# Kernel tuning notes

Measured on AMD Instinct MI355X. Metric: run time of the kernel, lower is better.

## Reference

```python
import jax, jax.numpy as jnp
import numpy as np

OBS, ACT, EMB, HID, NQ = 512, 32, 512, 512, 32
B = 32768


def setup_inputs() -> dict:
    key = jax.random.key(0)
    ks = jax.random.split(key, 12)
    s_in = 1.0 / np.sqrt(OBS + ACT)
    s_emb = 1.0 / np.sqrt(EMB)
    s_hid = 1.0 / np.sqrt(HID)
    return {
        "observation": jax.random.normal(ks[0], (B, OBS), jnp.float32),
        "prev_action": jax.random.normal(ks[1], (B, ACT), jnp.float32),
        "hidden_state": jax.random.normal(ks[2], (HID,), jnp.float32),
        "cell_state": jax.random.normal(ks[3], (HID,), jnp.float32),
        "W1": jax.random.uniform(ks[4], (EMB, OBS + ACT), jnp.float32, -s_in, s_in),
        "b1": jax.random.uniform(ks[5], (EMB,), jnp.float32, -s_in, s_in),
        "W_ih": jax.random.uniform(ks[6], (4 * HID, EMB), jnp.float32, -s_hid, s_hid),
        "b_ih": jax.random.uniform(ks[7], (4 * HID,), jnp.float32, -s_hid, s_hid),
        "W_hh": jax.random.uniform(ks[8], (4 * HID, HID), jnp.float32, -s_hid, s_hid),
        "b_hh": jax.random.uniform(ks[9], (4 * HID,), jnp.float32, -s_hid, s_hid),
        "W2": jax.random.uniform(ks[10], (NQ, HID), jnp.float32, -s_hid, s_hid),
        "b2": jax.random.uniform(ks[11], (NQ,), jnp.float32, -s_hid, s_hid),
    }


def reference(observation, prev_action, hidden_state, cell_state,
              W1, b1, W_ih, b_ih, W_hh, b_hh, W2, b2):
    # MLP1: Linear + ReLU over concat(obs, prev_action)  -> [B, EMB]
    x = jnp.concatenate([observation, prev_action], axis=-1)
    x = jax.nn.relu(x @ W1.T + b1)

    # Original torch code loops LSTMCell over batch, but reuses the SAME
    # (hidden_state, cell_state) every iteration -> fully batchable.
    # gates: [B, 4H]; h contribution is identical for all rows (broadcast).
    gates = x @ W_ih.T + b_ih + (hidden_state @ W_hh.T + b_hh)
    i, f, g, o = jnp.split(gates, 4, axis=-1)  # torch LSTMCell gate order
    i = jax.nn.sigmoid(i)
    f = jax.nn.sigmoid(f)
    g = jnp.tanh(g)
    o = jax.nn.sigmoid(o)
    c_new = f * cell_state + i * g          # [B, HID]
    h_new = o * jnp.tanh(c_new)             # [B, HID]

    q_values = h_new @ W2.T + b2             # [B, NQ]
    # torch returns last loop iteration's (h, c)
    return q_values, h_new[-1], c_new[-1]
```

## Files before the change

kernel.cpp:

```cpp
#include <hip/hip_runtime.h>
#include <stdint.h>

#define DEVINL __device__ __forceinline__

typedef __attribute__((ext_vector_type(8))) __bf16 bf16x8;
typedef __attribute__((ext_vector_type(4))) float f32x4;
typedef __attribute__((ext_vector_type(16))) float f32x16;
typedef __attribute__((ext_vector_type(4))) int i32x4;
typedef __attribute__((ext_vector_type(8))) int i32x8;

DEVINL unsigned short f2bf(float f) {
  union { float f; unsigned int u; } v; v.f = f;
  unsigned int u = v.u;
  return (unsigned short)((u + 0x7fffu + ((u >> 16) & 1u)) >> 16);
}

DEVINL unsigned char f2fp8(float f) {
  return (unsigned char)(__builtin_amdgcn_cvt_pk_fp8_f32(f, f, 0, false) & 0xff);
}

DEVINL float sigm(float x) { return __builtin_amdgcn_rcpf(1.f + __expf(-x)); }
DEVINL float tanh_(float x) {
  return 1.f - 2.f * __builtin_amdgcn_rcpf(1.f + __expf(2.f * x));
}

DEVINL size_t opt_off(int row, int k) {
  return (size_t)((row >> 5) * 8 + (k >> 6)) * 2048 + ((k >> 4) & 1) * 1024 +
         ((k >> 5) & 1) * 512 + (row & 31) * 16 + (k & 15);
}

#define GLD_LDS16(gptr, lptr)                                                  \
  __builtin_amdgcn_global_load_lds(                                            \
      (__attribute__((address_space(1))) void*)(gptr),                         \
      (__attribute__((address_space(3))) void*)(lptr), 16, 0, 0)

#define TOPBAR_6 asm volatile("s_waitcnt vmcnt(6) lgkmcnt(0)\n\ts_barrier" ::: "memory")
#define TOPBAR_4 asm volatile("s_waitcnt vmcnt(4) lgkmcnt(0)\n\ts_barrier" ::: "memory")
#define TOPBAR_1 asm volatile("s_waitcnt vmcnt(1) lgkmcnt(0)\n\ts_barrier" ::: "memory")
#define TOPBAR_0 asm volatile("s_waitcnt vmcnt(0) lgkmcnt(0)\n\ts_barrier" ::: "memory")
#define BOTBAR   asm volatile("s_waitcnt lgkmcnt(0)\n\ts_barrier" ::: "memory")

DEVINL int swz_col(int c) { return ((c & 3) ^ ((c >> 3) & 3)) * 8; }

__global__ void prep_all(const float* __restrict__ obs, const float* __restrict__ act,
                         const float* __restrict__ W1, const float* __restrict__ Wih,
                         const float* __restrict__ W2, const float* __restrict__ Whh,
                         const float* __restrict__ hid, const float* __restrict__ bhh,
                         const float* __restrict__ bih,
                         unsigned short* __restrict__ A0, unsigned short* __restrict__ W1b,
                         unsigned char* __restrict__ Wih8, unsigned short* __restrict__ W2b,
                         float* __restrict__ hvec) {
  const int bid = blockIdx.x, tid = threadIdx.x;
  if (bid < 2176) {
    const int total = 32768 * 68;
    for (int c = bid * 256 + tid; c < total; c += 2176 * 256) {
      const int b = c / 68, c8 = c % 68;
      const float* src = (c8 < 64) ? (obs + (size_t)b * 512 + c8 * 8)
                                   : (act + (size_t)b * 32 + (c8 - 64) * 8);
      float4 f0 = *(const float4*)src;
      float4 f1 = *(const float4*)(src + 4);
      unsigned short u[8] = {f2bf(f0.x), f2bf(f0.y), f2bf(f0.z), f2bf(f0.w),
                             f2bf(f1.x), f2bf(f1.y), f2bf(f1.z), f2bf(f1.w)};
      *(uint4*)(A0 + (size_t)b * 544 + c8 * 8) = *(uint4*)u;
    }
  } else if (bid < 2176 + 1312) {
    const int i = (bid - 2176) * 256 + tid;
    if (i < 69632) {
      float4 f = *(const float4*)(W1 + (size_t)i * 4);
      unsigned short u[4] = {f2bf(f.x), f2bf(f.y), f2bf(f.z), f2bf(f.w)};
      *(uint2*)(W1b + (size_t)i * 4) = *(uint2*)u;
    } else if (i < 69632 + 262144) {
      const int off = i - 69632;
      const int row = off >> 7, col0 = (off & 127) * 4;
      float4 f = *(const float4*)(Wih + (size_t)off * 4);
      int pk = __builtin_amdgcn_cvt_pk_fp8_f32(f.x * 16.f, f.y * 16.f, 0, false);
      pk = __builtin_amdgcn_cvt_pk_fp8_f32(f.z * 16.f, f.w * 16.f, pk, true);
      *(unsigned int*)(Wih8 + opt_off(row, col0)) = (unsigned int)pk;
    } else {
      const int off = i - 331776;
      float4 f = *(const float4*)(W2 + (size_t)off * 4);
      unsigned short u[4] = {f2bf(f.x), f2bf(f.y), f2bf(f.z), f2bf(f.w)};
      *(uint2*)(W2b + (size_t)off * 4) = *(uint2*)u;
    }
  } else {
    const int j = (bid - 3488) * 4 + (tid >> 6);
    const int lane = tid & 63;
    const float* w = Whh + (size_t)j * 512;
    float s = 0.f;
    for (int k = lane; k < 512; k += 64) s += w[k] * hid[k];
    for (int off = 32; off; off >>= 1) s += __shfl_down(s, off, 64);
    if (lane == 0) hvec[j] = s + bhh[j] + bih[j];
  }
}

__global__ __launch_bounds__(256, 2) void gemm1_relu(
    const unsigned short* __restrict__ A0,
    const unsigned short* __restrict__ W1b,
    const float* __restrict__ b1,
    unsigned char* __restrict__ X8) {
  constexpr int KT = 17, LD = 544;
  __shared__ __align__(16) unsigned short As[2][128 * 32];
  __shared__ __align__(16) unsigned short Bs[2][128 * 32];
  const int tid = threadIdx.x, wave = tid >> 6, lane = tid & 63;
  const int id = blockIdx.x, xcd = id & 7, slot = id >> 3;
  const int m0 = (xcd * 32 + (slot >> 2)) * 128;
  const int n0 = (slot & 3) * 128;
  const int wr = (wave >> 1) * 64, wc = (wave & 1) * 64;
  f32x4 acc[4][4] = {};

  const int c0 = tid, c1 = tid + 256;
  const unsigned short* pA0 = A0 + (size_t)(m0 + (c0 >> 2)) * LD + swz_col(c0);
  const unsigned short* pA1 = A0 + (size_t)(m0 + (c1 >> 2)) * LD + swz_col(c1);
  const unsigned short* pB0 = W1b + (size_t)(n0 + (c0 >> 2)) * LD + swz_col(c0);
  const unsigned short* pB1 = W1b + (size_t)(n0 + (c1 >> 2)) * LD + swz_col(c1);
  const int fr = lane & 15, q = lane >> 4;
  const int koff = (q ^ ((fr >> 1) & 3)) * 8;

#define STAGE1(buf)                                                            \
  do {                                                                         \
    GLD_LDS16(pA0, &As[(buf)][wave * 512]);                                    \
    GLD_LDS16(pA1, &As[(buf)][2048 + wave * 512]);                             \
    GLD_LDS16(pB0, &Bs[(buf)][wave * 512]);                                    \
    GLD_LDS16(pB1, &Bs[(buf)][2048 + wave * 512]);                             \
    pA0 += 32; pA1 += 32; pB0 += 32; pB1 += 32;                                \
  } while (0)

  STAGE1(0);
  for (int kt = 0; kt < KT; ++kt) {
    if (kt + 1 < KT) { STAGE1((kt + 1) & 1); TOPBAR_4; } else { TOPBAR_0; }
    const unsigned short* as = As[kt & 1];
    const unsigned short* bs = Bs[kt & 1];
    bf16x8 a[4], b[4];
#pragma unroll
    for (int i = 0; i < 4; ++i) a[i] = *(const bf16x8*)&as[(wr + i * 16 + fr) * 32 + koff];
#pragma unroll
    for (int j = 0; j < 4; ++j) b[j] = *(const bf16x8*)&bs[(wc + j * 16 + fr) * 32 + koff];
#pragma unroll
    for (int i = 0; i < 4; ++i)
#pragma unroll
      for (int j = 0; j < 4; ++j)
        acc[i][j] = __builtin_amdgcn_mfma_f32_16x16x32_bf16(a[i], b[j], acc[i][j], 0, 0, 0);
    BOTBAR;
  }
#undef STAGE1
  const int rbase = q * 4, cn = fr;
#pragma unroll
  for (int i = 0; i < 4; ++i)
#pragma unroll
    for (int j = 0; j < 4; ++j) {
      const int gn = n0 + wc + j * 16 + cn;
      const float bias = b1[gn];
#pragma unroll
      for (int r = 0; r < 4; ++r) {
        const int gm = m0 + wr + i * 16 + rbase + r;
        float v = acc[i][j][r] + bias;
        v = v > 0.f ? v : 0.f;
        X8[opt_off(gm, gn)] = f2fp8(v * 8.f);
      }
    }
}

__global__ __launch_bounds__(256, 2) void gemm2_lstm(
    const unsigned char* __restrict__ X8,
    const unsigned char* __restrict__ Wih8,
    const float* __restrict__ hvec,
    const float* __restrict__ cell,
    unsigned short* __restrict__ H,
    float* __restrict__ hlast,
    float* __restrict__ clast) {
  constexpr int KT = 8;
  __shared__ __align__(16) unsigned char As[2][256 * 64];
  __shared__ __align__(16) unsigned char Bs[2][4 * 32 * 64];
  const int tid = threadIdx.x, wave = tid >> 6, lane = tid & 63;
  const int id = blockIdx.x, xcd = id & 7, slot = id >> 3;
  const int m0 = (xcd * 16 + (slot >> 4)) * 256;
  const int n0 = (slot & 15) * 32;
  f32x16 acc00 = {}, acc01 = {}, acc02 = {}, acc03 = {};
  f32x16 acc10 = {}, acc11 = {}, acc12 = {}, acc13 = {};

  const int r31 = lane & 31, g2 = lane >> 5;
  const int fA = wave >> 1, hA = wave & 1;
  const unsigned char* pA0 = X8 + (size_t)((m0 >> 5) + 0 + fA) * 16384 + hA * 1024 + lane * 16;
  const unsigned char* pA1 = X8 + (size_t)((m0 >> 5) + 2 + fA) * 16384 + hA * 1024 + lane * 16;
  const unsigned char* pA2 = X8 + (size_t)((m0 >> 5) + 4 + fA) * 16384 + hA * 1024 + lane * 16;
  const unsigned char* pA3 = X8 + (size_t)((m0 >> 5) + 6 + fA) * 16384 + hA * 1024 + lane * 16;
  const unsigned char* pB0 =
      Wih8 + (size_t)((0 + fA) * 16 + (n0 >> 5)) * 16384 + hA * 1024 + lane * 16;
  const unsigned char* pB1 =
      Wih8 + (size_t)((2 + fA) * 16 + (n0 >> 5)) * 16384 + hA * 1024 + lane * 16;

  const int lb = lane * 16;

#define STAGE2(buf)                                                            \
  do {                                                                         \
    GLD_LDS16(pA0, &As[(buf)][wave * 1024]);                                   \
    GLD_LDS16(pA1, &As[(buf)][4096 + wave * 1024]);                            \
    GLD_LDS16(pA2, &As[(buf)][8192 + wave * 1024]);                            \
    GLD_LDS16(pA3, &As[(buf)][12288 + wave * 1024]);                           \
    GLD_LDS16(pB0, &Bs[(buf)][wave * 1024]);                                   \
    GLD_LDS16(pB1, &Bs[(buf)][4096 + wave * 1024]);                            \
    pA0 += 2048; pA1 += 2048; pA2 += 2048; pA3 += 2048;                        \
    pB0 += 2048; pB1 += 2048;                                                  \
  } while (0)

#define LDPAIR(dst, base_ptr, off)                                             \
  do {                                                                         \
    i32x4 lo_ = *(const i32x4*)((base_ptr) + (off) + lb);                      \
    i32x4 hi_ = *(const i32x4*)((base_ptr) + (off) + 1024 + lb);               \
    dst = __builtin_shufflevector(lo_, hi_, 0, 1, 2, 3, 4, 5, 6, 7);           \
  } while (0)

#define MFMA_MX(acc_, a_, b_)                                                  \
  acc_ = __builtin_amdgcn_mfma_scale_f32_32x32x64_f8f6f4(                      \
      a_, b_, acc_, 0, 0, 0, 0x7f7f7f7f, 0, 0x7f7f7f7f)

  STAGE2(0);
  for (int kt = 0; kt < KT; ++kt) {
    if (kt + 1 < KT) { STAGE2((kt + 1) & 1); TOPBAR_6; } else { TOPBAR_0; }
    const unsigned char* as = As[kt & 1];
    const unsigned char* bs = Bs[kt & 1];
    i32x8 b0, b1, b2, b3, a0, a1;
    LDPAIR(b0, bs, 0);
    LDPAIR(b1, bs, 2048);
    LDPAIR(b2, bs, 4096);
    LDPAIR(b3, bs, 6144);
    LDPAIR(a0, as, wave * 4096);
    LDPAIR(a1, as, wave * 4096 + 2048);
    MFMA_MX(acc00, a0, b0); MFMA_MX(acc01, a0, b1);
    MFMA_MX(acc02, a0, b2); MFMA_MX(acc03, a0, b3);
    MFMA_MX(acc10, a1, b0); MFMA_MX(acc11, a1, b1);
    MFMA_MX(acc12, a1, b2); MFMA_MX(acc13, a1, b3);
    BOTBAR;
  }
#undef STAGE2

  const int gn = n0 + r31;
  const float hv_i = hvec[gn];
  const float hv_f = hvec[gn + 512];
  const float hv_g = hvec[gn + 1024];
  const float hv_o = hvec[gn + 1536];
  const float cprev = cell[gn];
  constexpr float S = 1.f / 128.f;

#define EPILOG(F, ai, af, ag, ao)                                              \
  _Pragma("unroll")                                                            \
  for (int rg = 0; rg < 4; ++rg) {                                             \
    _Pragma("unroll")                                                          \
    for (int rr = 0; rr < 4; ++rr) {                                           \
      const int reg = rg * 4 + rr;                                             \
      const int gm = m0 + wave * 64 + (F) * 32 + rr + rg * 8 + g2 * 4;         \
      float si = sigm(ai[reg] * S + hv_i);                                     \
      float sf = sigm(af[reg] * S + hv_f);                                     \
      float tg = tanh_(ag[reg] * S + hv_g);                                    \
      float so = sigm(ao[reg] * S + hv_o);                                     \
      float cnew = sf * cprev + si * tg;                                       \
      float hnew = so * tanh_(cnew);                                           \
      H[(size_t)gm * 512 + gn] = f2bf(hnew);                                   \
      if (gm == 32767) { hlast[gn] = hnew; clast[gn] = cnew; }                 \
    }                                                                          \
  }

  EPILOG(0, acc00, acc01, acc02, acc03)
  EPILOG(1, acc10, acc11, acc12, acc13)
#undef EPILOG
#undef LDPAIR
#undef MFMA_MX
}

__global__ __launch_bounds__(256, 2) void gemm3(
    const unsigned short* __restrict__ H,
    const unsigned short* __restrict__ W2b,
    const float* __restrict__ b2,
    float* __restrict__ Q) {
  constexpr int KT = 16, LDW = 520;
  __shared__ __align__(16) unsigned short As[2][64 * 32];
  __shared__ __align__(16) unsigned short Ws[32 * LDW];
  const int tid = threadIdx.x, wave = tid >> 6, lane = tid & 63;
  const int id = blockIdx.x;
  const int m0 = ((id & 7) * 64 + (id >> 3)) * 64;
  for (int c = tid; c < 2048; c += 256) {
    const int row = c >> 6, col8 = c & 63;
    *(uint4*)&Ws[row * LDW + col8 * 8] = *(const uint4*)(W2b + row * 512 + col8 * 8);
  }
  f32x4 acc[2] = {};
  const int c0 = tid;
  const unsigned short* pA0 = H + (size_t)(m0 + (c0 >> 2)) * 512 + swz_col(c0);
  const int fr = lane & 15, q = lane >> 4;
  const int koff = (q ^ ((fr >> 1) & 3)) * 8;

#define STAGE3(buf)                                                            \
  do {                                                                         \
    GLD_LDS16(pA0, &As[(buf)][wave * 512]);                                    \
    pA0 += 32;                                                                 \
  } while (0)

  STAGE3(0);
  for (int kt = 0; kt < KT; ++kt) {
    if (kt + 1 < KT) { STAGE3((kt + 1) & 1); TOPBAR_1; } else { TOPBAR_0; }
    const unsigned short* as = As[kt & 1];
    const int k0 = kt * 32;
    bf16x8 a  = *(const bf16x8*)&as[(wave * 16 + fr) * 32 + koff];
    bf16x8 b0 = *(const bf16x8*)&Ws[fr * LDW + k0 + q * 8];
    bf16x8 b1 = *(const bf16x8*)&Ws[(16 + fr) * LDW + k0 + q * 8];
    acc[0] = __builtin_amdgcn_mfma_f32_16x16x32_bf16(a, b0, acc[0], 0, 0, 0);
    acc[1] = __builtin_amdgcn_mfma_f32_16x16x32_bf16(a, b1, acc[1], 0, 0, 0);
    BOTBAR;
  }
#undef STAGE3
  const int rbase = q * 4;
#pragma unroll
  for (int j = 0; j < 2; ++j) {
    const int gn = j * 16 + fr;
    const float bias = b2[gn];
#pragma unroll
    for (int r = 0; r < 4; ++r) {
      const int gm = m0 + wave * 16 + rbase + r;
      Q[(size_t)gm * 32 + gn] = acc[j][r] + bias;
    }
  }
}

extern "C" void kernel_launch(void* const* d_in, const int* in_sizes, int n_in,
                              void* d_out, int out_size, void* d_ws, size_t ws_size,
                              hipStream_t stream) {
  const float* obs  = (const float*)d_in[0];
  const float* act  = (const float*)d_in[1];
  const float* hid  = (const float*)d_in[2];
  const float* cell = (const float*)d_in[3];
  const float* W1   = (const float*)d_in[4];
  const float* b1   = (const float*)d_in[5];
  const float* Wih  = (const float*)d_in[6];
  const float* bih  = (const float*)d_in[7];
  const float* Whh  = (const float*)d_in[8];
  const float* bhh  = (const float*)d_in[9];
  const float* W2   = (const float*)d_in[10];
  const float* b2   = (const float*)d_in[11];
  float* out = (float*)d_out;

  char* ws = (char*)d_ws;
  unsigned short* A0   = (unsigned short*)(ws);
  unsigned short* H    = (unsigned short*)(ws);
  unsigned char*  X8   = (unsigned char*)(ws + 35651584);
  unsigned short* W1b  = (unsigned short*)(ws + 52428800);
  unsigned char*  Wih8 = (unsigned char*)(ws + 52985856);
  unsigned short* W2b  = (unsigned short*)(ws + 54034432);
  float*          hvec = (float*)(ws + 54067200);

  prep_all<<<4000, 256, 0, stream>>>(obs, act, W1, Wih, W2, Whh, hid, bhh, bih,
                                     A0, W1b, Wih8, W2b, hvec);
  gemm1_relu<<<1024, 256, 0, stream>>>(A0, W1b, b1, X8);
  gemm2_lstm<<<2048, 256, 0, stream>>>(X8, Wih8, hvec, cell, H,
                                       out + 32768 * 32,
                                       out + 32768 * 32 + 512);
  gemm3<<<512, 256, 0, stream>>>(H, W2b, b2, out);
}
```

Baseline: 212.4 us.

## Load LSTM GEMM operands directly from global into registers, dropping LDS staging

The gate GEMM kernel no longer stages A and B tiles through shared memory with async global-to-LDS copies and barriers. Each wave now loads its own A fragments and all four B fragments straight from global memory into registers, with register-level prefetch of the next A tile. This removes LDS traffic and per-iteration barriers, but B tiles are now fetched redundantly by every wave and global load latency is exposed more directly, relying on cache hits and occupancy to hide it.

After: 209.3 us. About the same (-1.5%).

```diff
diff --git a/kernel.cpp b/kernel.cpp
--- a/kernel.cpp
+++ b/kernel.cpp
@@ -34,7 +34,6 @@
       (__attribute__((address_space(1))) void*)(gptr),                         \
       (__attribute__((address_space(3))) void*)(lptr), 16, 0, 0)
 
-#define TOPBAR_6 asm volatile("s_waitcnt vmcnt(6) lgkmcnt(0)\n\ts_barrier" ::: "memory")
 #define TOPBAR_4 asm volatile("s_waitcnt vmcnt(4) lgkmcnt(0)\n\ts_barrier" ::: "memory")
 #define TOPBAR_1 asm volatile("s_waitcnt vmcnt(1) lgkmcnt(0)\n\ts_barrier" ::: "memory")
 #define TOPBAR_0 asm volatile("s_waitcnt vmcnt(0) lgkmcnt(0)\n\ts_barrier" ::: "memory")
@@ -168,45 +167,27 @@
     unsigned short* __restrict__ H,
     float* __restrict__ hlast,
     float* __restrict__ clast) {
-  constexpr int KT = 8;
-  __shared__ __align__(16) unsigned char As[2][256 * 64];
-  __shared__ __align__(16) unsigned char Bs[2][4 * 32 * 64];
   const int tid = threadIdx.x, wave = tid >> 6, lane = tid & 63;
   const int id = blockIdx.x, xcd = id & 7, slot = id >> 3;
   const int m0 = (xcd * 16 + (slot >> 4)) * 256;
   const int n0 = (slot & 15) * 32;
+  const int r31 = lane & 31, g2 = lane >> 5;
+  const int voff = g2 * 512 + r31 * 16;
+
   f32x16 acc00 = {}, acc01 = {}, acc02 = {}, acc03 = {};
   f32x16 acc10 = {}, acc11 = {}, acc12 = {}, acc13 = {};
 
-  const int r31 = lane & 31, g2 = lane >> 5;
-  const int fA = wave >> 1, hA = wave & 1;
-  const unsigned char* pA0 = X8 + (size_t)((m0 >> 5) + 0 + fA) * 16384 + hA * 1024 + lane * 16;
-  const unsigned char* pA1 = X8 + (size_t)((m0 >> 5) + 2 + fA) * 16384 + hA * 1024 + lane * 16;
-  const unsigned char* pA2 = X8 + (size_t)((m0 >> 5) + 4 + fA) * 16384 + hA * 1024 + lane * 16;
-  const unsigned char* pA3 = X8 + (size_t)((m0 >> 5) + 6 + fA) * 16384 + hA * 1024 + lane * 16;
-  const unsigned char* pB0 =
-      Wih8 + (size_t)((0 + fA) * 16 + (n0 >> 5)) * 16384 + hA * 1024 + lane * 16;
-  const unsigned char* pB1 =
-      Wih8 + (size_t)((2 + fA) * 16 + (n0 >> 5)) * 16384 + hA * 1024 + lane * 16;
-
-  const int lb = lane * 16;
-
-#define STAGE2(buf)                                                            \
+  const unsigned char* pa0 = X8 + (size_t)((m0 >> 5) + wave * 2 + 0) * 16384 + voff;
+  const unsigned char* pa1 = X8 + (size_t)((m0 >> 5) + wave * 2 + 1) * 16384 + voff;
+  const unsigned char* pb0 = Wih8 + (size_t)(0 * 16 + (n0 >> 5)) * 16384 + voff;
+  const unsigned char* pb1 = Wih8 + (size_t)(1 * 16 + (n0 >> 5)) * 16384 + voff;
+  const unsigned char* pb2 = Wih8 + (size_t)(2 * 16 + (n0 >> 5)) * 16384 + voff;
+  const unsigned char* pb3 = Wih8 + (size_t)(3 * 16 + (n0 >> 5)) * 16384 + voff;
+
+#define LD8(dst, p)                                                            \
   do {                                                                         \
-    GLD_LDS16(pA0, &As[(buf)][wave * 1024]);                                   \
-    GLD_LDS16(pA1, &As[(buf)][4096 + wave * 1024]);                            \
-    GLD_LDS16(pA2, &As[(buf)][8192 + wave * 1024]);                            \
-    GLD_LDS16(pA3, &As[(buf)][12288 + wave * 1024]);                           \
-    GLD_LDS16(pB0, &Bs[(buf)][wave * 1024]);                                   \
-    GLD_LDS16(pB1, &Bs[(buf)][4096 + wave * 1024]);                            \
-    pA0 += 2048; pA1 += 2048; pA2 += 2048; pA3 += 2048;                        \
-    pB0 += 2048; pB1 += 2048;                                                  \
-  } while (0)
-
-#define LDPAIR(dst, base_ptr, off)                                             \
-  do {                                                                         \
-    i32x4 lo_ = *(const i32x4*)((base_ptr) + (off) + lb);                      \
-    i32x4 hi_ = *(const i32x4*)((base_ptr) + (off) + 1024 + lb);               \
+    i32x4 lo_ = *(const i32x4*)(p);                                            \
+    i32x4 hi_ = *(const i32x4*)((p) + 1024);                                   \
     dst = __builtin_shufflevector(lo_, hi_, 0, 1, 2, 3, 4, 5, 6, 7);           \
   } while (0)
 
@@ -214,25 +195,24 @@
   acc_ = __builtin_amdgcn_mfma_scale_f32_32x32x64_f8f6f4(                      \
       a_, b_, acc_, 0, 0, 0, 0x7f7f7f7f, 0, 0x7f7f7f7f)
 
-  STAGE2(0);
-  for (int kt = 0; kt < KT; ++kt) {
-    if (kt + 1 < KT) { STAGE2((kt + 1) & 1); TOPBAR_6; } else { TOPBAR_0; }
-    const unsigned char* as = As[kt & 1];
-    const unsigned char* bs = Bs[kt & 1];
-    i32x8 b0, b1, b2, b3, a0, a1;
-    LDPAIR(b0, bs, 0);
-    LDPAIR(b1, bs, 2048);
-    LDPAIR(b2, bs, 4096);
-    LDPAIR(b3, bs, 6144);
-    LDPAIR(a0, as, wave * 4096);
-    LDPAIR(a1, as, wave * 4096 + 2048);
-    MFMA_MX(acc00, a0, b0); MFMA_MX(acc01, a0, b1);
-    MFMA_MX(acc02, a0, b2); MFMA_MX(acc03, a0, b3);
-    MFMA_MX(acc10, a1, b0); MFMA_MX(acc11, a1, b1);
-    MFMA_MX(acc12, a1, b2); MFMA_MX(acc13, a1, b3);
-    BOTBAR;
-  }
-#undef STAGE2
+  i32x8 A0, A1;
+  LD8(A0, pa0); LD8(A1, pa1);
+#pragma unroll
+  for (int kt = 0; kt < 8; ++kt) {
+    i32x8 B0, B1, B2, B3;
+    LD8(B0, pb0); LD8(B1, pb1); LD8(B2, pb2); LD8(B3, pb3);
+    pb0 += 2048; pb1 += 2048; pb2 += 2048; pb3 += 2048;
+    i32x8 nA0, nA1;
+    if (kt < 7) {
+      pa0 += 2048; pa1 += 2048;
+      LD8(nA0, pa0); LD8(nA1, pa1);
+    }
+    MFMA_MX(acc00, A0, B0); MFMA_MX(acc01, A0, B1);
+    MFMA_MX(acc02, A0, B2); MFMA_MX(acc03, A0, B3);
+    MFMA_MX(acc10, A1, B0); MFMA_MX(acc11, A1, B1);
+    MFMA_MX(acc12, A1, B2); MFMA_MX(acc13, A1, B3);
+    if (kt < 7) { A0 = nA0; A1 = nA1; }
+  }
 
   const int gn = n0 + r31;
   const float hv_i = hvec[gn];
@@ -263,7 +243,7 @@
   EPILOG(0, acc00, acc01, acc02, acc03)
   EPILOG(1, acc10, acc11, acc12, acc13)
 #undef EPILOG
-#undef LDPAIR
+#undef LD8
 #undef MFMA_MX
 }
 
```
